# Performance work log

Hardware: AMD Instinct MI355X
Metric: run time of the kernel (lower is better)

Reference implementation:

```python
import jax, jax.numpy as jnp
import numpy as np

B, N, F_IN, F_OUT, E = 8, 2048, 512, 256, 5
ALPHA = 0.2  # leaky relu slope
NEG = -9e15


def setup_inputs() -> dict:
    key = jax.random.key(0)
    ks = jax.random.split(key, 11)
    s_in = 1.0 / np.sqrt(F_IN)
    s_out = 1.0 / np.sqrt(F_OUT)
    s_e = 1.0 / np.sqrt(E)
    return {
        "feat": jax.random.normal(ks[0], (B, N, F_IN), jnp.float32),
        "adj": jax.random.randint(ks[1], (B, N, N), 0, 2, jnp.int32),
        "W": jax.random.normal(ks[2], (F_IN, F_OUT), jnp.float32) * s_in,
        "W_1": jax.random.normal(ks[3], (F_IN, F_OUT), jnp.float32) * s_in,
        "W_2": jax.random.normal(ks[4], (F_IN, F_OUT), jnp.float32) * s_in,
        "a_1": jax.random.normal(ks[5], (F_OUT, 1), jnp.float32) * s_out,
        "a_2": jax.random.normal(ks[6], (F_OUT, 1), jnp.float32) * s_out,
        "a_12": jax.random.normal(ks[7], (F_OUT, F_OUT), jnp.float32) * s_out,
        "L_w": jax.random.normal(ks[8], (E, F_IN), jnp.float32) * s_in,
        "R_w": jax.random.normal(ks[9], (E, F_IN), jnp.float32) * s_in,
        "B_w": jax.random.normal(ks[10], (F_OUT, E, E), jnp.float32) * s_e,
    }


def reference(feat, adj, W, W_1, W_2, a_1, a_2, a_12, L_w, R_w, B_w):
    # --- attention ---
    h = jnp.einsum('bnf,fd->bnd', feat, W)                 # [B,N,D]
    Ax = jnp.einsum('bnd,do->bno', h, a_1)[..., 0]         # [B,N] (score of target)
    Ay = jnp.einsum('bnd,do->bno', h, a_2)[..., 0]         # [B,N] (score of source)
    A_xy = jnp.einsum('bid,de,bje->bij', h, a_12, h)       # [B,N,N] bilinear term
    logits = Ax[:, None, :] + Ay[:, :, None] + A_xy        # [B,N,N]
    e = jnp.where(logits > 0, logits, ALPHA * logits)      # leaky relu
    e = jnp.where(adj > 0, e, NEG)
    attention = jax.nn.softmax(e, axis=-1)                 # dropout p=0 / eval -> identity
    # --- aggregate ---
    feat_agg = jnp.einsum('bij,bjf->bif', attention, feat) # [B,N,F_IN]
    # --- update ---
    h_1 = jnp.einsum('bnf,fd->bnd', feat, W_1)
    h_2 = jnp.einsum('bnf,fd->bnd', feat_agg, W_2)
    e1 = jnp.einsum('bnf,ef->bne', feat, L_w)              # [B,N,E]
    e2 = jnp.einsum('bnf,ef->bne', feat_agg, R_w)          # [B,N,E]
    h_12 = jnp.einsum('bni,oij,bnj->bno', e1, B_w, e2)     # [B,N,F_OUT]
    return h_1 + h_2 + h_12  # activation=None -> identity
```

## Files before the change

kernel.cpp:

```cpp
#include <hip/hip_runtime.h>
#include <hip/hip_bf16.h>

#define BB 8
#define NN 2048
#define FIN 512
#define FOUT 256
#define EE 5
#define ALPHA_ 0.2f
#define NEGV -9e15f
#define JW 512

typedef __hip_bfloat16 bf16;
typedef __bf16 bf16x8 __attribute__((ext_vector_type(8)));
typedef float f32x4 __attribute__((ext_vector_type(4)));
typedef unsigned long long u64;

__device__ __forceinline__ float bf2f(bf16 x) { return __bfloat162float(x); }
__device__ __forceinline__ bf16 f2bf(float x) { return __float2bfloat16(x); }

__device__ __forceinline__ void async16(const bf16* g, bf16* l) {
    __builtin_amdgcn_global_load_lds(
        (const __attribute__((address_space(1))) void*)g,
        (__attribute__((address_space(3))) void*)l, 16, 0, 0);
}

__global__ void split_f32_bf16(const float* __restrict__ in,
                               bf16* __restrict__ hi, bf16* __restrict__ lo) {
    long i = ((long)blockIdx.x * blockDim.x + threadIdx.x) * 8;
    float4 a = *(const float4*)(&in[i]);
    float4 b = *(const float4*)(&in[i + 4]);
    float x[8] = { a.x, a.y, a.z, a.w, b.x, b.y, b.z, b.w };
    bf16 th[8], tl[8];
    for (int k = 0; k < 8; k++) {
        th[k] = f2bf(x[k]);
        tl[k] = f2bf(x[k] - bf2f(th[k]));
    }
    *(uint4*)(&hi[i]) = *(const uint4*)th;
    *(uint4*)(&lo[i]) = *(const uint4*)tl;
}

__global__ void pack_adj(const int* __restrict__ adj, u64* __restrict__ adjm) {
    long wid = (((long)blockIdx.x * 256) + threadIdx.x) >> 6;
    int lane = threadIdx.x & 63;
    long base = wid * 256;
    for (int c = 0; c < 4; c++) {
        int a = adj[base + c * 64 + lane];
        u64 m = __ballot(a > 0);
        if (lane == 0) adjm[base / 64 + c] = m;
    }
}

__global__ void transpose_split(const float* __restrict__ in,
                                bf16* __restrict__ hi, bf16* __restrict__ lo,
                                int R, int C) {
    __shared__ bf16 th[32][33], tl[32][33];
    int c0 = blockIdx.x * 32, r0 = blockIdx.y * 32;
    int x = threadIdx.x, y = threadIdx.y;
    for (int k = 0; k < 4; k++) {
        int r = y + k * 8;
        float f = in[(long)(r0 + r) * C + c0 + x];
        bf16 h = f2bf(f);
        th[r][x] = h;
        tl[r][x] = f2bf(f - bf2f(h));
    }
    __syncthreads();
    for (int k = 0; k < 4; k++) {
        int r = y + k * 8;
        hi[(long)(c0 + r) * R + r0 + x] = th[x][r];
        lo[(long)(c0 + r) * R + r0 + x] = tl[x][r];
    }
}

__global__ void transpose_f32_bf16(const float* __restrict__ in, bf16* __restrict__ out,
                                   int R, int C, long sin_b, long sout_b) {
    __shared__ bf16 tile[32][33];
    long bi = (long)blockIdx.z * sin_b;
    long bo = (long)blockIdx.z * sout_b;
    int c0 = blockIdx.x * 32, r0 = blockIdx.y * 32;
    int x = threadIdx.x, y = threadIdx.y;
    for (int k = 0; k < 4; k++) {
        int r = y + k * 8;
        tile[r][x] = f2bf(in[bi + (long)(r0 + r) * C + c0 + x]);
    }
    __syncthreads();
    for (int k = 0; k < 4; k++) {
        int r = y + k * 8;
        out[bo + (long)(c0 + r) * R + r0 + x] = tile[x][r];
    }
}

__global__ __launch_bounds__(256) void gemm_bt_split(
        const bf16* __restrict__ Ah, const bf16* __restrict__ Al,
        const bf16* __restrict__ Bh, const bf16* __restrict__ Bl,
        bf16* __restrict__ Chi, bf16* __restrict__ Clo,
        const float* __restrict__ bias, int Nn, int K) {
    __shared__ alignas(16) bf16 Ash[128 * 32], Asl[128 * 32];
    __shared__ alignas(16) bf16 Bsh[128 * 32], Bsl[128 * 32];
    int tid = threadIdx.x;
    int lane = tid & 63, ww = tid >> 6;
    int wm = ww >> 1, wn = ww & 1;
    int quad = lane >> 4, l16 = lane & 15;
    int m0 = blockIdx.x * 128, n0 = blockIdx.y * 128;
    f32x4 acc[4][4] = {};
    for (int k0 = 0; k0 < K; k0 += 32) {
#pragma unroll
        for (int i = 0; i < 2; i++) {
            int idx = tid + i * 256;
            int row = idx >> 2, seg = idx & 3;
            long ao = (long)(m0 + row) * K + k0 + seg * 8;
            long bo = (long)(n0 + row) * K + k0 + seg * 8;
            async16(&Ah[ao], &Ash[idx * 8]);
            async16(&Al[ao], &Asl[idx * 8]);
            async16(&Bh[bo], &Bsh[idx * 8]);
            async16(&Bl[bo], &Bsl[idx * 8]);
        }
        __syncthreads();
        bf16x8 afh[4], afl[4], bfh[4], bfl[4];
        for (int mi = 0; mi < 4; mi++) {
            int so = (wm * 64 + mi * 16 + l16) * 32 + quad * 8;
            afh[mi] = *(const bf16x8*)(&Ash[so]);
            afl[mi] = *(const bf16x8*)(&Asl[so]);
        }
        for (int ni = 0; ni < 4; ni++) {
            int so = (wn * 64 + ni * 16 + l16) * 32 + quad * 8;
            bfh[ni] = *(const bf16x8*)(&Bsh[so]);
            bfl[ni] = *(const bf16x8*)(&Bsl[so]);
        }
        for (int mi = 0; mi < 4; mi++)
            for (int ni = 0; ni < 4; ni++) {
                acc[mi][ni] = __builtin_amdgcn_mfma_f32_16x16x32_bf16(afh[mi], bfh[ni], acc[mi][ni], 0, 0, 0);
                acc[mi][ni] = __builtin_amdgcn_mfma_f32_16x16x32_bf16(afh[mi], bfl[ni], acc[mi][ni], 0, 0, 0);
                acc[mi][ni] = __builtin_amdgcn_mfma_f32_16x16x32_bf16(afl[mi], bfh[ni], acc[mi][ni], 0, 0, 0);
            }
        __syncthreads();
    }
    for (int mi = 0; mi < 4; mi++)
        for (int ni = 0; ni < 4; ni++) {
            int col = n0 + wn * 64 + ni * 16 + l16;
            float bv = bias ? bias[col] : 0.f;
            for (int r = 0; r < 4; r++) {
                int row = m0 + wm * 64 + mi * 16 + quad * 4 + r;
                float v = acc[mi][ni][r] + bv;
                bf16 h = f2bf(v);
                Chi[(long)row * Nn + col] = h;
                Clo[(long)row * Nn + col] = f2bf(v - bf2f(h));
            }
        }
}

__global__ __launch_bounds__(256) void gemm_bt(
        const bf16* __restrict__ A, const bf16* __restrict__ Bt,
        bf16* __restrict__ C, int Nn, int K, long sA, long sB, long sC) {
    __shared__ alignas(16) bf16 As[128 * 32];
    __shared__ alignas(16) bf16 Bs[128 * 32];
    const bf16* Ab = A + (long)blockIdx.z * sA;
    const bf16* Bb = Bt + (long)blockIdx.z * sB;
    bf16* Cb = C + (long)blockIdx.z * sC;
    int tid = threadIdx.x;
    int lane = tid & 63, ww = tid >> 6;
    int wm = ww >> 1, wn = ww & 1;
    int quad = lane >> 4, l16 = lane & 15;
    int m0 = blockIdx.x * 128, n0 = blockIdx.y * 128;
    f32x4 acc[4][4] = {};
    for (int k0 = 0; k0 < K; k0 += 32) {
#pragma unroll
        for (int i = 0; i < 2; i++) {
            int idx = tid + i * 256;
            int row = idx >> 2, seg = idx & 3;
            async16(&Ab[(long)(m0 + row) * K + k0 + seg * 8], &As[idx * 8]);
            async16(&Bb[(long)(n0 + row) * K + k0 + seg * 8], &Bs[idx * 8]);
        }
        __syncthreads();
        bf16x8 af[4], bfr[4];
        for (int mi = 0; mi < 4; mi++)
            af[mi] = *(const bf16x8*)(&As[(wm * 64 + mi * 16 + l16) * 32 + quad * 8]);
        for (int ni = 0; ni < 4; ni++)
            bfr[ni] = *(const bf16x8*)(&Bs[(wn * 64 + ni * 16 + l16) * 32 + quad * 8]);
        for (int mi = 0; mi < 4; mi++)
            for (int ni = 0; ni < 4; ni++)
                acc[mi][ni] = __builtin_amdgcn_mfma_f32_16x16x32_bf16(
                    af[mi], bfr[ni], acc[mi][ni], 0, 0, 0);
        __syncthreads();
    }
    for (int mi = 0; mi < 4; mi++)
        for (int ni = 0; ni < 4; ni++) {
            int col = n0 + wn * 64 + ni * 16 + l16;
            for (int r = 0; r < 4; r++) {
                int row = m0 + wm * 64 + mi * 16 + quad * 4 + r;
                Cb[(long)row * Nn + col] = f2bf(acc[mi][ni][r]);
            }
        }
}

__global__ void ay_kernel(const bf16* __restrict__ hh, const bf16* __restrict__ hl,
                          const float* __restrict__ a2, float* __restrict__ Ay) {
    int lane = threadIdx.x & 63, w = threadIdx.x >> 6;
    long row = (long)blockIdx.x * 4 + w;
    float p = 0.f;
    for (int i = 0; i < 4; i++) {
        int d = i * 64 + lane;
        p += (bf2f(hh[row * FOUT + d]) + bf2f(hl[row * FOUT + d])) * a2[d];
    }
    for (int off = 32; off; off >>= 1) p += __shfl_xor(p, off);
    if (lane == 0) Ay[row] = p;
}

__global__ __launch_bounds__(256) void pass_score(
        const bf16* __restrict__ qh_, const bf16* __restrict__ ql_,
        const bf16* __restrict__ hh_, const bf16* __restrict__ hl_,
        const u64* __restrict__ adjm, const float* __restrict__ Ay,
        float* __restrict__ mpm, float* __restrict__ mpl,
        bf16* __restrict__ P) {
    __shared__ alignas(16) bf16 Hsh[128 * 32], Hsl[128 * 32];
    __shared__ alignas(16) bf16 pst[4][16 * 128];
    int tid = threadIdx.x;
    int lane = tid & 63, w = tid >> 6;
    int quad = lane >> 4, l16 = lane & 15;
    int b = blockIdx.z, jz = blockIdx.y;
    int i0 = blockIdx.x * 64 + w * 16;
    long qoff = ((long)b * NN + i0) * FOUT;
    const bf16* hbh = hh_ + ((long)b * NN + (long)jz * JW) * FOUT;
    const bf16* hbl = hl_ + ((long)b * NN + (long)jz * JW) * FOUT;
    const u64* amb = adjm + ((long)b * NN + i0) * (NN / 64) + jz * (JW / 64);
    bf16* pw = pst[w];

    bf16x8 qfh[8], qfl[8];
#pragma unroll
    for (int kk = 0; kk < 8; kk++) {
        qfh[kk] = *(const bf16x8*)(&qh_[qoff + (long)l16 * FOUT + kk * 32 + quad * 8]);
        qfl[kk] = *(const bf16x8*)(&ql_[qoff + (long)l16 * FOUT + kk * 32 + quad * 8]);
    }
    float ay_[4];
#pragma unroll
    for (int r = 0; r < 4; r++) ay_[r] = Ay[(long)b * NN + i0 + quad * 4 + r];

    float m_[4], l_[4];
#pragma unroll
    for (int r = 0; r < 4; r++) { m_[r] = -3.0e38f; l_[r] = 0.f; }

    for (int jc = 0; jc < JW / 128; jc++) {
        f32x4 sacc[8] = {};
#pragma unroll
        for (int kk = 0; kk < 8; kk++) {
            __syncthreads();
#pragma unroll
            for (int i = 0; i < 2; i++) {
                int idx = tid + i * 256;
                int row = idx >> 2, seg = idx & 3;
                long go = (long)(jc * 128 + row) * FOUT + kk * 32 + seg * 8;
                async16(&hbh[go], &Hsh[idx * 8]);
                async16(&hbl[go], &Hsl[idx * 8]);
            }
            __syncthreads();
#pragma unroll
            for (int ni = 0; ni < 8; ni++) {
                int so = (ni * 16 + l16) * 32 + quad * 8;
                bf16x8 hfh = *(const bf16x8*)(&Hsh[so]);
                bf16x8 hfl = *(const bf16x8*)(&Hsl[so]);
                sacc[ni] = __builtin_amdgcn_mfma_f32_16x16x32_bf16(qfh[kk], hfh, sacc[ni], 0, 0, 0);
                sacc[ni] = __builtin_amdgcn_mfma_f32_16x16x32_bf16(qfh[kk], hfl, sacc[ni], 0, 0, 0);
                sacc[ni] = __builtin_amdgcn_mfma_f32_16x16x32_bf16(qfl[kk], hfh, sacc[ni], 0, 0, 0);
            }
        }
        u64 am[4][2];
#pragma unroll
        for (int r = 0; r < 4; r++) {
            am[r][0] = amb[(long)(quad * 4 + r) * (NN / 64) + jc * 2 + 0];
            am[r][1] = amb[(long)(quad * 4 + r) * (NN / 64) + jc * 2 + 1];
        }
#pragma unroll
        for (int ni = 0; ni < 8; ni++)
#pragma unroll
            for (int r = 0; r < 4; r++) {
                float v = sacc[ni][r] + ay_[r];
                v = v > 0.f ? v : ALPHA_ * v;
                int bit = (int)((am[r][ni >> 2] >> ((ni * 16 + l16) & 63)) & 1);
                sacc[ni][r] = bit ? v : NEGV;
            }
#pragma unroll
        for (int r = 0; r < 4; r++) {
            float mc = -3.0e38f;
#pragma unroll
            for (int ni = 0; ni < 8; ni++) mc = fmaxf(mc, sacc[ni][r]);
            for (int off = 8; off; off >>= 1) mc = fmaxf(mc, __shfl_xor(mc, off));
            float mnew = fmaxf(m_[r], mc);
            float scale = __expf(m_[r] - mnew);
            float ps = 0.f;
#pragma unroll
            for (int ni = 0; ni < 8; ni++) {
                float p = __expf(sacc[ni][r] - mnew);
                sacc[ni][r] = p;
                ps += p;
            }
            for (int off = 8; off; off >>= 1) ps += __shfl_xor(ps, off);
            l_[r] = l_[r] * scale + ps;
            m_[r] = mnew;
            if (l16 == 0)
                mpm[(((long)b * 4 + jz) * 4 + jc) * NN + i0 + quad * 4 + r] = mnew;
        }
#pragma unroll
        for (int ni = 0; ni < 8; ni++)
#pragma unroll
            for (int r = 0; r < 4; r++)
                pw[(quad * 4 + r) * 128 + ni * 16 + l16] = f2bf(sacc[ni][r]);
#pragma unroll
        for (int s2 = 0; s2 < 4; s2++) {
            int seg = quad * 4 + s2;
            uint4 v = *(const uint4*)(&pw[l16 * 128 + seg * 8]);
            *(uint4*)(&P[((long)b * NN + i0 + l16) * NN + jz * JW + jc * 128 + seg * 8]) = v;
        }
    }
    if (l16 == 0)
#pragma unroll
        for (int r = 0; r < 4; r++)
            mpl[((long)b * 4 + jz) * NN + i0 + quad * 4 + r] = l_[r];
}

__global__ void ml_merge(const float* __restrict__ mpm, const float* __restrict__ mpl,
                         float2* __restrict__ mlfin) {
    long row = (long)blockIdx.x * blockDim.x + threadIdx.x;
    long b = row / NN, n = row % NN;
    float mw[4];
    float m = -3.0e38f;
    for (int jz = 0; jz < 4; jz++) {
        mw[jz] = mpm[((b * 4 + jz) * 4 + 3) * NN + n];
        m = fmaxf(m, mw[jz]);
    }
    float l = 0.f;
    for (int jz = 0; jz < 4; jz++)
        l += mpl[(b * 4 + jz) * NN + n] * __expf(mw[jz] - m);
    mlfin[row] = make_float2(m, 1.f / l);
}

__global__ __launch_bounds__(256) void fixup_p(
        bf16* __restrict__ P, const float* __restrict__ mpm,
        const float2* __restrict__ mlfin) {
    int row = blockIdx.x, b = blockIdx.y;
    int t = threadIdx.x;
    int jz = t >> 6, jc = (t >> 4) & 3;
    float2 mf = mlfin[(long)b * NN + row];
    float scale = __expf(mpm[(((long)b * 4 + jz) * 4 + jc) * NN + row] - mf.x) * mf.y;
    long base = ((long)b * NN + row) * NN + t * 8;
    uint4 v = *(const uint4*)(&P[base]);
    bf16* pv = (bf16*)&v;
    bf16 o[8];
    for (int k = 0; k < 8; k++) o[k] = f2bf(bf2f(pv[k]) * scale);
    *(uint4*)(&P[base]) = *(const uint4*)o;
}

__global__ void e_kernel(const bf16* __restrict__ X, const float* __restrict__ Wt,
                         float* __restrict__ out) {
    int lane = threadIdx.x & 63, w = threadIdx.x >> 6;
    long row = (long)blockIdx.x * 4 + w;
    uint4 raw = *(const uint4*)(&X[row * FIN + lane * 8]);
    const bf16* xp = (const bf16*)&raw;
    float xv[8];
    for (int i = 0; i < 8; i++) xv[i] = bf2f(xp[i]);
    for (int e = 0; e < EE; e++) {
        float4 w0 = *(const float4*)(&Wt[e * FIN + lane * 8]);
        float4 w1 = *(const float4*)(&Wt[e * FIN + lane * 8 + 4]);
        float p = xv[0] * w0.x + xv[1] * w0.y + xv[2] * w0.z + xv[3] * w0.w
                + xv[4] * w1.x + xv[5] * w1.y + xv[6] * w1.z + xv[7] * w1.w;
        for (int off = 32; off; off >>= 1) p += __shfl_xor(p, off);
        if (lane == 0) out[row * EE + e] = p;
    }
}

__global__ void final_kernel(float* __restrict__ out,
                             const bf16* __restrict__ h1, const bf16* __restrict__ h2,
                             const float* __restrict__ e1, const float* __restrict__ e2,
                             const float* __restrict__ Bw) {
    long row = blockIdx.x;
    int o = threadIdx.x;
    float a[EE], c[EE];
    for (int i = 0; i < EE; i++) { a[i] = e1[row * EE + i]; c[i] = e2[row * EE + i]; }
    const float* bw = Bw + (long)o * EE * EE;
    float acc = 0.f;
    for (int i = 0; i < EE; i++)
        for (int j = 0; j < EE; j++)
            acc += bw[i * EE + j] * a[i] * c[j];
    long idx = row * FOUT + o;
    out[idx] = acc + bf2f(h1[idx]) + bf2f(h2[idx]);
}

extern "C" void kernel_launch(void* const* d_in, const int* in_sizes, int n_in,
                              void* d_out, int out_size, void* d_ws, size_t ws_size,
                              hipStream_t stream) {
    const float* feat = (const float*)d_in[0];
    const int*   adj  = (const int*)d_in[1];
    const float* W    = (const float*)d_in[2];
    const float* W1   = (const float*)d_in[3];
    const float* W2   = (const float*)d_in[4];
    const float* a1   = (const float*)d_in[5];
    const float* a2   = (const float*)d_in[6];
    const float* a12  = (const float*)d_in[7];
    const float* Lw   = (const float*)d_in[8];
    const float* Rw   = (const float*)d_in[9];
    const float* Bw   = (const float*)d_in[10];
    float* out = (float*)d_out;

    char* ws = (char*)d_ws;
    size_t off = 0;
    auto alloc = [&](size_t bytes) {
        char* p = ws + off;
        off += (bytes + 255) & ~(size_t)255;
        return p;
    };
    bf16* WTh  = (bf16*)alloc((size_t)FOUT * FIN * 2);
    bf16* WTl  = (bf16*)alloc((size_t)FOUT * FIN * 2);
    bf16* W1T  = (bf16*)alloc((size_t)FOUT * FIN * 2);
    bf16* W2T  = (bf16*)alloc((size_t)FOUT * FIN * 2);
    bf16* aTh  = (bf16*)alloc((size_t)FOUT * FOUT * 2);
    bf16* aTl  = (bf16*)alloc((size_t)FOUT * FOUT * 2);
    bf16* fh   = (bf16*)alloc((size_t)BB * NN * FIN * 2);
    bf16* fl   = (bf16*)alloc((size_t)BB * NN * FIN * 2);
    bf16* hh   = (bf16*)alloc((size_t)BB * NN * FOUT * 2);
    bf16* hl   = (bf16*)alloc((size_t)BB * NN * FOUT * 2);
    bf16* featT= (bf16*)alloc((size_t)BB * NN * FIN * 2);
    float* Ay  = (float*)alloc((size_t)BB * NN * 4);
    float* mpm = (float*)alloc((size_t)BB * 4 * 4 * NN * 4);
    float* mpl = (float*)alloc((size_t)BB * 4 * NN * 4);
    float2* mlfin = (float2*)alloc((size_t)BB * NN * 8);
    float* e1  = (float*)alloc((size_t)BB * NN * EE * 4);
    float* e2  = (float*)alloc((size_t)BB * NN * EE * 4);
    u64* adjm  = (u64*)alloc((size_t)BB * NN * (NN / 64) * 8);
    bf16* P    = (bf16*)alloc((size_t)BB * NN * NN * 2);
    bf16* qh   = (bf16*)d_out;
    bf16* ql   = qh + (size_t)BB * NN * FOUT;
    bf16* fagg = fl;
    bf16* h1   = hh;
    bf16* h2   = hl;

    dim3 tb(32, 8, 1);
    split_f32_bf16<<<(BB * NN * FIN) / (256 * 8), 256, 0, stream>>>(feat, fh, fl);
    pack_adj<<<(BB * NN * NN) / (256 * 4), 256, 0, stream>>>(adj, adjm);
    transpose_split<<<dim3(FOUT / 32, FIN / 32, 1), tb, 0, stream>>>(W, WTh, WTl, FIN, FOUT);
    transpose_split<<<dim3(FOUT / 32, FOUT / 32, 1), tb, 0, stream>>>(a12, aTh, aTl, FOUT, FOUT);
    transpose_f32_bf16<<<dim3(FOUT / 32, FIN / 32, 1), tb, 0, stream>>>(W1, W1T, FIN, FOUT, 0, 0);
    transpose_f32_bf16<<<dim3(FOUT / 32, FIN / 32, 1), tb, 0, stream>>>(W2, W2T, FIN, FOUT, 0, 0);
    transpose_f32_bf16<<<dim3(FIN / 32, NN / 32, BB), tb, 0, stream>>>(
        feat, featT, NN, FIN, (long)NN * FIN, (long)FIN * NN);
    gemm_bt_split<<<dim3(BB * NN / 128, FOUT / 128, 1), 256, 0, stream>>>(
        fh, fl, WTh, WTl, hh, hl, nullptr, FOUT, FIN);
    ay_kernel<<<BB * NN / 4, 256, 0, stream>>>(hh, hl, a2, Ay);
    gemm_bt_split<<<dim3(BB * NN / 128, FOUT / 128, 1), 256, 0, stream>>>(
        hh, hl, aTh, aTl, qh, ql, a1, FOUT, FOUT);
    pass_score<<<dim3(NN / 64, 4, BB), 256, 0, stream>>>(
        qh, ql, hh, hl, adjm, Ay, mpm, mpl, P);
    ml_merge<<<(BB * NN) / 256, 256, 0, stream>>>(mpm, mpl, mlfin);
    fixup_p<<<dim3(NN, BB, 1), 256, 0, stream>>>(P, mpm, mlfin);
    gemm_bt<<<dim3(NN / 128, FIN / 128, BB), 256, 0, stream>>>(
        P, featT, fagg, FIN, NN, (long)NN * NN, (long)FIN * NN, (long)NN * FIN);
    gemm_bt<<<dim3(BB * NN / 128, FOUT / 128, 1), 256, 0, stream>>>(
        fh, W1T, h1, FOUT, FIN, 0, 0, 0);
    gemm_bt<<<dim3(BB * NN / 128, FOUT / 128, 1), 256, 0, stream>>>(
        fagg, W2T, h2, FOUT, FIN, 0, 0, 0);
    e_kernel<<<BB * NN / 4, 256, 0, stream>>>(fh, Lw, e1);
    e_kernel<<<BB * NN / 4, 256, 0, stream>>>(fagg, Rw, e2);
    final_kernel<<<BB * NN, FOUT, 0, stream>>>(out, h1, h2, e1, e2, Bw);
}
```

Measured before the change: 553.4 us.

## Double-buffer H tiles in pass_score with async prefetch and swizzled P staging

Reworks the pass_score main loop into one flat 32-stage loop that prefetches the next H tile into a second LDS buffer while the current one feeds the MFMAs, using explicit vmcnt waits and barriers. It also raises MFMA wave priority, adds an occupancy hint through launch_bounds, and halves the P staging buffer, writing it with an XOR swizzle in two halves to avoid LDS bank conflicts. The aim is to hide global-to-LDS load latency and raise occupancy. In exchange it uses more LDS for the H tiles and relies on hand-tuned waitcnt counts being correct.

```diff
diff --git a/kernel.cpp b/kernel.cpp
--- a/kernel.cpp
+++ b/kernel.cpp
@@ -205,14 +205,14 @@
     if (lane == 0) Ay[row] = p;
 }
 
-__global__ __launch_bounds__(256) void pass_score(
+__global__ __launch_bounds__(256, 4) void pass_score(
         const bf16* __restrict__ qh_, const bf16* __restrict__ ql_,
         const bf16* __restrict__ hh_, const bf16* __restrict__ hl_,
         const u64* __restrict__ adjm, const float* __restrict__ Ay,
         float* __restrict__ mpm, float* __restrict__ mpl,
         bf16* __restrict__ P) {
-    __shared__ alignas(16) bf16 Hsh[128 * 32], Hsl[128 * 32];
-    __shared__ alignas(16) bf16 pst[4][16 * 128];
+    __shared__ alignas(16) bf16 Hsh[2][128 * 32], Hsl[2][128 * 32];
+    __shared__ alignas(16) bf16 pst[4][16 * 64];
     int tid = threadIdx.x;
     int lane = tid & 63, w = tid >> 6;
     int quad = lane >> 4, l16 = lane & 15;
@@ -238,77 +238,105 @@
 #pragma unroll
     for (int r = 0; r < 4; r++) { m_[r] = -3.0e38f; l_[r] = 0.f; }
 
-    for (int jc = 0; jc < JW / 128; jc++) {
-        f32x4 sacc[8] = {};
-#pragma unroll
-        for (int kk = 0; kk < 8; kk++) {
-            __syncthreads();
-#pragma unroll
-            for (int i = 0; i < 2; i++) {
-                int idx = tid + i * 256;
-                int row = idx >> 2, seg = idx & 3;
-                long go = (long)(jc * 128 + row) * FOUT + kk * 32 + seg * 8;
-                async16(&hbh[go], &Hsh[idx * 8]);
-                async16(&hbl[go], &Hsl[idx * 8]);
-            }
-            __syncthreads();
-#pragma unroll
-            for (int ni = 0; ni < 8; ni++) {
-                int so = (ni * 16 + l16) * 32 + quad * 8;
-                bf16x8 hfh = *(const bf16x8*)(&Hsh[so]);
-                bf16x8 hfl = *(const bf16x8*)(&Hsl[so]);
-                sacc[ni] = __builtin_amdgcn_mfma_f32_16x16x32_bf16(qfh[kk], hfh, sacc[ni], 0, 0, 0);
-                sacc[ni] = __builtin_amdgcn_mfma_f32_16x16x32_bf16(qfh[kk], hfl, sacc[ni], 0, 0, 0);
-                sacc[ni] = __builtin_amdgcn_mfma_f32_16x16x32_bf16(qfl[kk], hfh, sacc[ni], 0, 0, 0);
-            }
-        }
-        u64 am[4][2];
-#pragma unroll
-        for (int r = 0; r < 4; r++) {
-            am[r][0] = amb[(long)(quad * 4 + r) * (NN / 64) + jc * 2 + 0];
-            am[r][1] = amb[(long)(quad * 4 + r) * (NN / 64) + jc * 2 + 1];
-        }
-#pragma unroll
-        for (int ni = 0; ni < 8; ni++)
+    auto STAGE = [&](int s, int buf) {
+        int jc = s >> 3, kk = s & 7;
+#pragma unroll
+        for (int i = 0; i < 2; i++) {
+            int idx = tid + i * 256;
+            int row = idx >> 2, seg = idx & 3;
+            long go = (long)(jc * 128 + row) * FOUT + kk * 32 + seg * 8;
+            async16(&hbh[go], &Hsh[buf][idx * 8]);
+            async16(&hbl[go], &Hsl[buf][idx * 8]);
+        }
+    };
+
+    f32x4 sacc[8];
+#pragma unroll
+    for (int ni = 0; ni < 8; ni++) sacc[ni] = (f32x4){0.f, 0.f, 0.f, 0.f};
+
+    STAGE(0, 0);
+    for (int s = 0; s < 32; s++) {
+        int kk = s & 7, jc = s >> 3, cur = s & 1;
+        if (s + 1 < 32) STAGE(s + 1, cur ^ 1);
+        __builtin_amdgcn_sched_barrier(0);
+        if (s + 1 < 32) asm volatile("s_waitcnt vmcnt(4)" ::: "memory");
+        else            asm volatile("s_waitcnt vmcnt(0)" ::: "memory");
+        __builtin_amdgcn_s_barrier();
+        __builtin_amdgcn_sched_barrier(0);
+
+        __builtin_amdgcn_s_setprio(1);
+#pragma unroll
+        for (int ni = 0; ni < 8; ni++) {
+            int so = (ni * 16 + l16) * 32 + quad * 8;
+            bf16x8 hfh = *(const bf16x8*)(&Hsh[cur][so]);
+            bf16x8 hfl = *(const bf16x8*)(&Hsl[cur][so]);
+            sacc[ni] = __builtin_amdgcn_mfma_f32_16x16x32_bf16(qfh[kk], hfh, sacc[ni], 0, 0, 0);
+            sacc[ni] = __builtin_amdgcn_mfma_f32_16x16x32_bf16(qfh[kk], hfl, sacc[ni], 0, 0, 0);
+            sacc[ni] = __builtin_amdgcn_mfma_f32_16x16x32_bf16(qfl[kk], hfh, sacc[ni], 0, 0, 0);
+        }
+        __builtin_amdgcn_s_setprio(0);
+
+        if (kk == 7) {
+            u64 am[4][2];
 #pragma unroll
             for (int r = 0; r < 4; r++) {
-                float v = sacc[ni][r] + ay_[r];
-                v = v > 0.f ? v : ALPHA_ * v;
-                int bit = (int)((am[r][ni >> 2] >> ((ni * 16 + l16) & 63)) & 1);
-                sacc[ni][r] = bit ? v : NEGV;
-            }
-#pragma unroll
-        for (int r = 0; r < 4; r++) {
-            float mc = -3.0e38f;
-#pragma unroll
-            for (int ni = 0; ni < 8; ni++) mc = fmaxf(mc, sacc[ni][r]);
-            for (int off = 8; off; off >>= 1) mc = fmaxf(mc, __shfl_xor(mc, off));
-            float mnew = fmaxf(m_[r], mc);
-            float scale = __expf(m_[r] - mnew);
-            float ps = 0.f;
-#pragma unroll
-            for (int ni = 0; ni < 8; ni++) {
-                float p = __expf(sacc[ni][r] - mnew);
-                sacc[ni][r] = p;
-                ps += p;
-            }
-            for (int off = 8; off; off >>= 1) ps += __shfl_xor(ps, off);
-            l_[r] = l_[r] * scale + ps;
-            m_[r] = mnew;
-            if (l16 == 0)
-                mpm[(((long)b * 4 + jz) * 4 + jc) * NN + i0 + quad * 4 + r] = mnew;
-        }
-#pragma unroll
-        for (int ni = 0; ni < 8; ni++)
-#pragma unroll
-            for (int r = 0; r < 4; r++)
-                pw[(quad * 4 + r) * 128 + ni * 16 + l16] = f2bf(sacc[ni][r]);
-#pragma unroll
-        for (int s2 = 0; s2 < 4; s2++) {
-            int seg = quad * 4 + s2;
-            uint4 v = *(const uint4*)(&pw[l16 * 128 + seg * 8]);
-            *(uint4*)(&P[((long)b * NN + i0 + l16) * NN + jz * JW + jc * 128 + seg * 8]) = v;
-        }
+                am[r][0] = amb[(long)(quad * 4 + r) * (NN / 64) + jc * 2 + 0];
+                am[r][1] = amb[(long)(quad * 4 + r) * (NN / 64) + jc * 2 + 1];
+            }
+#pragma unroll
+            for (int ni = 0; ni < 8; ni++)
+#pragma unroll
+                for (int r = 0; r < 4; r++) {
+                    float v = sacc[ni][r] + ay_[r];
+                    v = v > 0.f ? v : ALPHA_ * v;
+                    int bit = (int)((am[r][ni >> 2] >> ((ni * 16 + l16) & 63)) & 1);
+                    sacc[ni][r] = bit ? v : NEGV;
+                }
+#pragma unroll
+            for (int r = 0; r < 4; r++) {
+                float mc = -3.0e38f;
+#pragma unroll
+                for (int ni = 0; ni < 8; ni++) mc = fmaxf(mc, sacc[ni][r]);
+                for (int off = 8; off; off >>= 1) mc = fmaxf(mc, __shfl_xor(mc, off));
+                float mnew = fmaxf(m_[r], mc);
+                float scale = __expf(m_[r] - mnew);
+                float ps = 0.f;
+#pragma unroll
+                for (int ni = 0; ni < 8; ni++) {
+                    float p = __expf(sacc[ni][r] - mnew);
+                    sacc[ni][r] = p;
+                    ps += p;
+                }
+                for (int off = 8; off; off >>= 1) ps += __shfl_xor(ps, off);
+                l_[r] = l_[r] * scale + ps;
+                m_[r] = mnew;
+                if (l16 == 0)
+                    mpm[(((long)b * 4 + jz) * 4 + jc) * NN + i0 + quad * 4 + r] = mnew;
+            }
+#pragma unroll
+            for (int h = 0; h < 2; h++) {
+#pragma unroll
+                for (int ni = 0; ni < 4; ni++)
+#pragma unroll
+                    for (int r = 0; r < 4; r++) {
+                        int row = quad * 4 + r;
+                        int byt = (row * 128 + (ni * 16 + l16) * 2) ^ ((row & 7) << 4);
+                        *(bf16*)((char*)pw + byt) = f2bf(sacc[h * 4 + ni][r]);
+                    }
+#pragma unroll
+                for (int s2 = 0; s2 < 2; s2++) {
+                    int cq = quad + s2 * 4;
+                    int byt = (l16 * 128 + cq * 16) ^ ((l16 & 7) << 4);
+                    uint4 v = *(const uint4*)((const char*)pw + byt);
+                    *(uint4*)(&P[((long)b * NN + i0 + l16) * NN + (long)jz * JW
+                                 + jc * 128 + h * 64 + cq * 8]) = v;
+                }
+            }
+#pragma unroll
+            for (int ni = 0; ni < 8; ni++) sacc[ni] = (f32x4){0.f, 0.f, 0.f, 0.f};
+        }
+        __builtin_amdgcn_sched_barrier(0);
+        __builtin_amdgcn_s_barrier();
     }
     if (l16 == 0)
 #pragma unroll
```

Result: slower. 959.7 us (+73.4%).
